# Optimization experiments

Hardware: AMD Instinct MI355X
Metric: run time of the kernel (lower is better)

The kernel has to match this reference:

```python
import jax, jax.numpy as jnp
import numpy as np
from jax import lax

H = 128       # hidden_size
N = 128       # total agents
T = 12        # future_steps (hardcoded by .view(12, ...))
K = 20        # num_modes
NHEADS = 4
HD = H // NHEADS
MIN_SCALE = 0.001


def setup_inputs() -> dict:
    key = jax.random.key(0)
    ks = jax.random.split(key, 48)

    def w(i, shape, fan):
        return (jax.random.normal(ks[i], shape, dtype=jnp.float32) / np.float32(np.sqrt(fan)))

    z = lambda *s: jnp.zeros(s, jnp.float32)
    o = lambda *s: jnp.ones(s, jnp.float32)
    inp = {}
    inp['global_embed'] = jax.random.normal(ks[0], (T, N, H), dtype=jnp.float32)
    inp['hidden_state'] = jax.random.normal(ks[1], (N, H), dtype=jnp.float32)
    inp['cn'] = jax.random.normal(ks[2], (N, H), dtype=jnp.float32)
    inp['shift_values'] = jax.random.normal(ks[3], (1, N, 2), dtype=jnp.float32)
    inp['max_values'] = jax.random.uniform(ks[4], (N, 2), dtype=jnp.float32)
    # multihead_proj_global: Linear(H, K*H) + LayerNorm + ReLU
    inp['mhp_W'] = w(5, (H, K * H), H); inp['mhp_b'] = z(K * H)
    inp['mhp_g'] = o(K * H); inp['mhp_beta'] = z(K * H)
    # two LSTMCells (bias = b_ih + b_hh fused)
    inp['lstm1_Wih'] = w(6, (H, 4 * H), H); inp['lstm1_Whh'] = w(7, (H, 4 * H), H); inp['lstm1_b'] = z(4 * H)
    inp['lstm2_Wih'] = w(8, (H, 4 * H), H); inp['lstm2_Whh'] = w(9, (H, 4 * H), H); inp['lstm2_b'] = z(4 * H)
    # MultiHeadSelfAttention
    inp['Wq'] = w(10, (H, H), H); inp['bq'] = z(H)
    inp['Wk'] = w(11, (H, H), H); inp['bk'] = z(H)
    inp['Wv'] = w(12, (H, H), H); inp['bv'] = z(H)
    inp['Wo1'] = w(13, (H, 2 * H), H); inp['bo1'] = z(2 * H)
    inp['Wo2'] = w(14, (2 * H, H), 2 * H); inp['bo2'] = z(H)
    # loc head: Linear + LN + ReLU + Linear(H,2)
    inp['loc_W1'] = w(15, (H, H), H); inp['loc_b1'] = z(H)
    inp['loc_g'] = o(H); inp['loc_beta'] = z(H)
    inp['loc_W2'] = w(16, (H, 2), H); inp['loc_b2'] = z(2)
    # scale head
    inp['scl_W1'] = w(17, (H, H), H); inp['scl_b1'] = z(H)
    inp['scl_g'] = o(H); inp['scl_beta'] = z(H)
    inp['scl_W2'] = w(18, (H, 2), H); inp['scl_b2'] = z(2)
    inp['batch_split'] = 4  # number of equal scene segments
    return inp


def _ln(x, g, b):
    m = jnp.mean(x, -1, keepdims=True)
    v = jnp.mean((x - m) ** 2, -1, keepdims=True)
    return (x - m) / jnp.sqrt(v + 1e-5) * g + b


def _head(x, W1, b1, g, beta, W2, b2):
    return jax.nn.relu(_ln(x @ W1 + b1, g, beta)) @ W2 + b2


def reference(global_embed, hidden_state, cn, shift_values, max_values,
              mhp_W, mhp_b, mhp_g, mhp_beta,
              lstm1_Wih, lstm1_Whh, lstm1_b,
              lstm2_Wih, lstm2_Whh, lstm2_b,
              Wq, bq, Wk, bk, Wv, bv, Wo1, bo1, Wo2, bo2,
              loc_W1, loc_b1, loc_g, loc_beta, loc_W2, loc_b2,
              scl_W1, scl_b1, scl_g, scl_beta, scl_W2, scl_b2,
              batch_split):
    S = int(batch_split)
    n = N // S
    # project global embed to per-mode embeddings: [T,N,K*H] -> [T,K*N,H] (mode-major)
    ge = jax.nn.relu(_ln(global_embed @ mhp_W + mhp_b, mhp_g, mhp_beta))
    ge = ge.reshape(T, N, K, H).transpose(0, 2, 1, 3).reshape(T, K * N, H)
    h0 = jnp.tile(hidden_state, (K, 1))  # [K*N,H]
    c0 = jnp.tile(cn, (K, 1))

    def cell1(carry, x):
        h, c = carry
        gi, gf, gg, go = jnp.split(x @ lstm1_Wih + h @ lstm1_Whh + lstm1_b, 4, -1)
        c2 = jax.nn.sigmoid(gf) * c + jax.nn.sigmoid(gi) * jnp.tanh(gg)
        h2 = jax.nn.sigmoid(go) * jnp.tanh(c2)
        return (h2, c2), h2

    _, output1 = lax.scan(cell1, (h0, c0), ge)  # [T,K*N,H]

    loc1 = _head(output1, loc_W1, loc_b1, loc_g, loc_beta, loc_W2, loc_b2)
    loc1 = loc1.transpose(1, 0, 2).reshape(K, N, T, 2)
    scale1 = jax.nn.elu(_head(output1, scl_W1, scl_b1, scl_g, scl_beta, scl_W2, scl_b2)) + 1.0 + MIN_SCALE
    scale1 = scale1.transpose(1, 0, 2).reshape(K, N, T, 2)

    sv = shift_values[0]  # squeeze(0) -> [N,2]
    loc1_ = loc1 * max_values[:, None, :] + sv[:, None, :]            # [K,N,T,2]
    loc1_ = loc1_.transpose(0, 2, 1, 3).reshape(K * T, N, 2).transpose(0, 2, 1)  # [K*T,2,N]
    locs = loc1_.reshape(K * T, 2, S, n).transpose(2, 0, 1, 3)        # [S,K*T,2,n]

    def split_mask(x):  # x: [K*T,2,n]
        d = jnp.abs(x[:, :, :, None] - x[:, :, None, :])              # [K*T,2,n,n]
        m = ((d[:, 0] < 10.0) & (d[:, 1] < 10.0)).reshape(K, T, n, n).any(0)  # [T,n,n]
        return jnp.tile(m, (1, K, K))                                  # [T,K*n,K*n]

    masks = jax.vmap(split_mask)(locs)  # [S,T,K*n,K*n]

    o1d = lax.stop_gradient(output1)  # detach, as in torch
    o1d = o1d.reshape(T, K, S, n, H).transpose(2, 0, 1, 3, 4).reshape(S, T, K * n, H)

    def mhsa(x, mask):  # x: [T,L,H], mask: [T,L,L] bool
        L = K * n
        q = (x @ Wq + bq).reshape(T, L, NHEADS, HD)
        k = (x @ Wk + bk).reshape(T, L, NHEADS, HD)
        v = (x @ Wv + bv).reshape(T, L, NHEADS, HD)
        s = jnp.einsum('blhd,bmhd->bhlm', q, k) / np.float32(np.sqrt(HD))
        s = jnp.where(mask[:, None], s, jnp.float32(-1e8))
        ctx = jnp.einsum('bhlm,bmhd->blhd', jax.nn.softmax(s, -1), v).reshape(T, L, H)
        return jax.nn.relu(ctx @ Wo1 + bo1) @ Wo2 + bo2

    social = jax.vmap(mhsa)(o1d, masks)                                # [S,T,K*n,H]
    social = social.reshape(S, T, K, n, H).transpose(1, 2, 0, 3, 4).reshape(T, K * N, H)

    def cell2(carry, xs):
        h, c = carry
        x, soc = xs
        c = c + soc
        h = h + jnp.tanh(c)
        gi, gf, gg, go = jnp.split(x @ lstm2_Wih + h @ lstm2_Whh + lstm2_b, 4, -1)
        c2 = jax.nn.sigmoid(gf) * c + jax.nn.sigmoid(gi) * jnp.tanh(gg)
        h2 = jax.nn.sigmoid(go) * jnp.tanh(c2)
        return (h2, c2), h2

    _, output2 = lax.scan(cell2, (h0, c0), (ge, social))  # [T,K*N,H]

    loc2 = _head(output2, loc_W1, loc_b1, loc_g, loc_beta, loc_W2, loc_b2)
    loc2 = loc2.transpose(1, 0, 2).reshape(K, N, T, 2)
    scale2 = jax.nn.elu(_head(output2, scl_W1, scl_b1, scl_g, scl_beta, scl_W2, scl_b2)) + 1.0 + MIN_SCALE
    scale2 = scale2.transpose(1, 0, 2).reshape(K, N, T, 2)

    return jnp.stack([loc1, scale1, loc2, scale2], 0)  # [4,K,N,T,2]
```

## Files before the change

kernel.cpp:

```cpp
#include <hip/hip_runtime.h>
#include <hip/hip_bf16.h>

typedef __hip_bfloat16 bf16_t;

static const int cT  = 12;
static const int cN  = 128;
static const int cH  = 128;
static const int cK  = 20;
static const int cKN = 2560;
static const int cS  = 4;
static const int cNS = 32;
static const int cL  = 640;
static const int cHD = 32;

#define CONV_TOTAL 977986

__constant__ int c_off[38] = {0,196608,212992,229376,229632,229888,557568,560128,562688,
  565248,630784,696320,696832,762368,827904,828416,844800,844928,861312,861440,877824,
  877952,910720,910976,943744,943872,960256,960384,960512,960640,960896,960960,977344,
  977472,977600,977728,977984,977986};
__constant__ int c_len[37] = {196608,16384,16384,256,256,327680,2560,2560,2560,
  65536,65536,512,65536,65536,512,16384,128,16384,128,16384,128,
  32768,256,32768,128,16384,128,128,128,256,2,16384,128,128,128,256,2};

struct Ptrs { const void* p[37]; };

typedef __attribute__((ext_vector_type(4))) float f32x4;
typedef __attribute__((ext_vector_type(8))) __bf16 bf16x8;

__device__ __forceinline__ float sigm(float x){ return 1.f/(1.f+expf(-x)); }
__device__ __forceinline__ unsigned short f2h(float x){ return (unsigned short)(__float_as_uint(x)>>16); }
__device__ __forceinline__ float hif(float x){ return __uint_as_float(__float_as_uint(x)&0xFFFF0000u); }

__global__ __launch_bounds__(256) void k_detect(const unsigned short* ge_u16, int* flagp, unsigned int* outw){
  __shared__ int cnt;
  if (threadIdx.x == 0) cnt = 0;
  __syncthreads();
  int ok = 0;
  for (int i = threadIdx.x; i < 128; i += 64){
    unsigned short u = ge_u16[2*i];
    int ex = (u >> 7) & 0xFF;
    if (ex >= 100 && ex <= 140) ok++;
  }
  atomicAdd(&cnt, ok);
  __syncthreads();
  if (threadIdx.x == 0){
    *flagp = (cnt >= 96) ? 1 : 0;
    outw[0] = 0x7FC07FC0u;
  }
}

__global__ __launch_bounds__(256) void k_convert(Ptrs ptrs, const int* flagp, float* dst){
  int g = blockIdx.x*256 + threadIdx.x;
  if (g >= CONV_TOTAL) return;
  int flag = *flagp;
  int seg = 0;
  while (seg < 36 && g >= c_off[seg+1]) ++seg;
  int local = g - c_off[seg];
  if (local >= c_len[seg]) return;
  float v;
  if (flag) v = __bfloat162float(((const bf16_t*)ptrs.p[seg])[local]);
  else      v = ((const float*)ptrs.p[seg])[local];
  dst[g] = v;
}

__global__ __launch_bounds__(256) void k_wprep3(const float* W, unsigned short* out){
  int idx = blockIdx.x*256 + threadIdx.x;
  int l = idx & 63;
  int rest = idx >> 6;
  int s = rest & 3;
  int n = rest >> 2;
  int g = l >> 4, c16 = l & 15;
  unsigned short hi[8], lo[8];
  #pragma unroll
  for (int e = 0; e < 8; ++e){
    int k = 32*s + 16*(e>>2) + 4*g + (e&3);
    float v = W[k*2560 + 16*n + c16];
    hi[e] = f2h(v); lo[e] = f2h(v - hif(v));
  }
  size_t base = (size_t)idx*8;
  *(uint4*)&out[base]          = *(const uint4*)hi;
  *(uint4*)&out[base + 327680] = *(const uint4*)lo;
}

__global__ __launch_bounds__(256) void k_mhp_ln(const float* y, const float* g,
                      const float* be, float* out){
  int row = blockIdx.x;
  int tid = threadIdx.x;
  __shared__ float red[256];
  float v[10];
  const float* yr = y + (size_t)row*2560;
  #pragma unroll
  for (int m = 0; m < 10; ++m) v[m] = yr[tid + 256*m];
  float ps = 0.f;
  #pragma unroll
  for (int m = 0; m < 10; ++m) ps += v[m];
  red[tid] = ps; __syncthreads();
  for (int s2 = 128; s2 > 0; s2 >>= 1){
    if (tid < s2) red[tid] += red[tid+s2];
    __syncthreads();
  }
  float mean = red[0]*(1.f/2560.f);
  __syncthreads();
  float pv = 0.f;
  #pragma unroll
  for (int m = 0; m < 10; ++m){ float d = v[m]-mean; pv += d*d; }
  red[tid] = pv; __syncthreads();
  for (int s2 = 128; s2 > 0; s2 >>= 1){
    if (tid < s2) red[tid] += red[tid+s2];
    __syncthreads();
  }
  float inv = rsqrtf(red[0]*(1.f/2560.f) + 1e-5f);
  int t = row >> 7, nn = row & 127;
  #pragma unroll
  for (int m = 0; m < 10; ++m){
    int col = tid + 256*m;
    float z = (v[m]-mean)*inv*g[col] + be[col];
    z = fmaxf(z, 0.f);
    int k = col >> 7, hh2 = col & 127;
    out[((t*cKN) + k*cN + nn)*cH + hh2] = z;
  }
}

__global__ __launch_bounds__(256) void k_wprep(const float* w0, const float* w1,
    const float* w2, const float* w3, unsigned short* out){
  int idx = blockIdx.x*256 + threadIdx.x;
  int m = idx >> 13;
  int rest = idx & 8191;
  int n = rest >> 8;
  int s = (rest >> 6) & 3;
  int l = rest & 63;
  int g = l >> 4, c16 = l & 15;
  const float* W = (m==0) ? w0 : ((m==1) ? w1 : ((m==2) ? w2 : w3));
  unsigned short hi[8], lo[8];
  #pragma unroll
  for (int e = 0; e < 8; ++e){
    int k = 32*s + 16*(e>>2) + 4*g + (e&3);
    float v = W[k*512 + 16*n + c16];
    hi[e] = f2h(v); lo[e] = f2h(v - hif(v));
  }
  size_t base = (size_t)m*131072 + (size_t)((n*4 + s)*64 + l)*8;
  *(uint4*)&out[base]         = *(const uint4*)hi;
  *(uint4*)&out[base + 65536] = *(const uint4*)lo;
}

__global__ __launch_bounds__(256) void k_wprep2(const float* wq, const float* wk,
    const float* wv, const float* wo1, const float* wo2,
    unsigned short* outA, unsigned short* outB){
  int idx = blockIdx.x*256 + threadIdx.x;
  if (idx >= 14336) return;
  const float* W; int KF, N, local, half; unsigned short* out; size_t off;
  if (idx < 2048)      { W=wq;  KF=4; N=128; off=0;      local=idx;       half=16384; out=outA; }
  else if (idx < 4096) { W=wk;  KF=4; N=128; off=32768;  local=idx-2048;  half=16384; out=outA; }
  else if (idx < 6144) { W=wv;  KF=4; N=128; off=65536;  local=idx-4096;  half=16384; out=outA; }
  else if (idx < 10240){ W=wo1; KF=4; N=256; off=98304;  local=idx-6144;  half=32768; out=outA; }
  else                 { W=wo2; KF=8; N=128; off=0;      local=idx-10240; half=32768; out=outB; }
  int l = local & 63;
  int rest = local >> 6;
  int s = rest & (KF-1);
  int n = (KF == 8) ? (rest >> 3) : (rest >> 2);
  int g = l >> 4, c16 = l & 15;
  unsigned short hi[8], lo[8];
  #pragma unroll
  for (int e = 0; e < 8; ++e){
    int k = 32*s + 16*(e>>2) + 4*g + (e&3);
    float v = W[k*N + 16*n + c16];
    hi[e] = f2h(v); lo[e] = f2h(v - hif(v));
  }
  size_t base = off + (size_t)local*8;
  *(uint4*)&out[base]        = *(const uint4*)hi;
  *(uint4*)&out[base + half] = *(const uint4*)lo;
}

__global__ __launch_bounds__(512) void k_lstm_mfma(const float* ge, float* outh,
    const float* hs0, const float* cn0, const float* soc,
    const unsigned short* wfA, const unsigned short* wfB,
    const float* bias, int phase){
  int r0 = blockIdx.x * 16;
  int tid = threadIdx.x;
  int w = tid >> 6, l = tid & 63;
  int g = l >> 4, c16 = l & 15;
  int scol = w*16 + c16;
  __shared__ unsigned short HFh[2][4][64][8], HFl[2][4][64][8];
  int ps = scol >> 5, prem = scol & 31;
  int pgf = (prem >> 2) & 3;
  int pe  = ((prem >> 4) << 2) + (prem & 3);
  float c[4], h[4];
  #pragma unroll
  for (int r = 0; r < 4; ++r){
    int nn = (r0 + 4*g + r) & 127;
    c[r] = cn0[nn*cH + scol];
    h[r] = hs0[nn*cH + scol];
  }
  float bias_t[4];
  #pragma unroll
  for (int tt = 0; tt < 4; ++tt) bias_t[tt] = bias[tt*128 + scol];

  f32x4 xr[8];
  float socr[4] = {0.f, 0.f, 0.f, 0.f};
  {
    const f32x4* gp = (const f32x4*)ge + ((size_t)(r0 + c16))*32;
    #pragma unroll
    for (int s = 0; s < 4; ++s){ xr[2*s] = gp[8*s + g]; xr[2*s+1] = gp[8*s + 4 + g]; }
    if (phase == 2){
      #pragma unroll
      for (int r = 0; r < 4; ++r)
        socr[r] = soc[(size_t)(r0 + 4*g + r)*cH + scol];
    }
  }

  for (int t = 0; t < cT; ++t){
    int b = t & 1;
    if (phase == 2){
      #pragma unroll
      for (int r = 0; r < 4; ++r){
        c[r] += socr[r];
        h[r] += tanhf(c[r]);
      }
    }
    #pragma unroll
    for (int r = 0; r < 4; ++r){
      HFh[b][ps][pgf*16 + 4*g + r][pe] = f2h(h[r]);
      HFl[b][ps][pgf*16 + 4*g + r][pe] = f2h(h[r] - hif(h[r]));
    }
    bf16x8 xh[4], xl[4];
    #pragma unroll
    for (int s = 0; s < 4; ++s){
      union { unsigned short u[8]; bf16x8 v; } uh, ul;
      #pragma unroll
      for (int m2 = 0; m2 < 4; ++m2){
        float a0 = xr[2*s][m2], b0 = xr[2*s+1][m2];
        uh.u[m2]   = f2h(a0); ul.u[m2]   = f2h(a0 - hif(a0));
        uh.u[4+m2] = f2h(b0); ul.u[4+m2] = f2h(b0 - hif(b0));
      }
      xh[s] = uh.v; xl[s] = ul.v;
    }
    if (t < cT-1){
      const f32x4* gp = (const f32x4*)ge + ((size_t)(t+1)*cKN + r0 + c16)*32;
      #pragma unroll
      for (int s = 0; s < 4; ++s){ xr[2*s] = gp[8*s + g]; xr[2*s+1] = gp[8*s + 4 + g]; }
      if (phase == 2){
        #pragma unroll
        for (int r = 0; r < 4; ++r)
          socr[r] = soc[(size_t)(t+1)*cKN*cH + (size_t)(r0 + 4*g + r)*cH + scol];
      }
    }
    __syncthreads();
    bf16x8 hh[4], hl[4];
    #pragma unroll
    for (int s = 0; s < 4; ++s){
      hh[s] = *(const bf16x8*)&HFh[b][s][l][0];
      hl[s] = *(const bf16x8*)&HFl[b][s][l][0];
    }
    f32x4 a4[4];
    #pragma unroll
    for (int tt = 0; tt < 4; ++tt){
      f32x4 acc = {bias_t[tt], bias_t[tt], bias_t[tt], bias_t[tt]};
      a4[tt] = acc;
    }
    {
      bf16x8 cAh, cAl, cBh, cBl, nAh, nAl, nBh, nBl;
      {
        size_t fo = (size_t)((w*4 + 0)*64 + l)*8;
        cAh = *(const bf16x8*)&wfA[fo];
        cAl = *(const bf16x8*)&wfA[65536 + fo];
        cBh = *(const bf16x8*)&wfB[fo];
        cBl = *(const bf16x8*)&wfB[65536 + fo];
      }
      #pragma unroll
      for (int j = 0; j < 16; ++j){
        int s = j >> 2, tt = j & 3;
        if (j < 15){
          int j2 = j + 1;
          int s2 = j2 >> 2, tt2 = j2 & 3;
          size_t fo = (size_t)(((w + 8*tt2)*4 + s2)*64 + l)*8;
          nAh = *(const bf16x8*)&wfA[fo];
          nAl = *(const bf16x8*)&wfA[65536 + fo];
          nBh = *(const bf16x8*)&wfB[fo];
          nBl = *(const bf16x8*)&wfB[65536 + fo];
        }
        f32x4 acc = a4[tt];
        acc = __builtin_amdgcn_mfma_f32_16x16x32_bf16(xl[s], cAh, acc, 0, 0, 0);
        acc = __builtin_amdgcn_mfma_f32_16x16x32_bf16(xh[s], cAl, acc, 0, 0, 0);
        acc = __builtin_amdgcn_mfma_f32_16x16x32_bf16(xh[s], cAh, acc, 0, 0, 0);
        acc = __builtin_amdgcn_mfma_f32_16x16x32_bf16(hl[s], cBh, acc, 0, 0, 0);
        acc = __builtin_amdgcn_mfma_f32_16x16x32_bf16(hh[s], cBl, acc, 0, 0, 0);
        acc = __builtin_amdgcn_mfma_f32_16x16x32_bf16(hh[s], cBh, acc, 0, 0, 0);
        a4[tt] = acc;
        cAh = nAh; cAl = nAl; cBh = nBh; cBl = nBl;
      }
    }
    #pragma unroll
    for (int r = 0; r < 4; ++r){
      float ig = sigm(a4[0][r]), fg = sigm(a4[1][r]);
      float gg = tanhf(a4[2][r]), og = sigm(a4[3][r]);
      c[r] = fg*c[r] + ig*gg;
      h[r] = og*tanhf(c[r]);
      outh[(size_t)t*cKN*cH + (size_t)(r0 + 4*g + r)*cH + scol] = h[r];
    }
  }
}

template<int KF>
__global__ __launch_bounds__(256) void k_gemm(const float* x, const unsigned short* wf,
    const float* bias, float* out, int NT, int N, int relu, int half, int ntc){
  int r0 = blockIdx.x * 16;
  int nt0 = blockIdx.y * ntc;
  int ntEnd = nt0 + ntc; if (ntEnd > NT) ntEnd = NT;
  int tid = threadIdx.x;
  int wv = tid >> 6, l = tid & 63;
  int g = l >> 4, c16 = l & 15;
  bf16x8 xh[KF], xl[KF];
  const f32x4* gp = (const f32x4*)x + (size_t)(r0 + c16)*(KF*8);
  #pragma unroll
  for (int s = 0; s < KF; ++s){
    f32x4 qa = gp[8*s + g], qb = gp[8*s + 4 + g];
    union { unsigned short u[8]; bf16x8 v; } uh, ul;
    #pragma unroll
    for (int m2 = 0; m2 < 4; ++m2){
      float a0 = qa[m2], b0 = qb[m2];
      uh.u[m2]   = f2h(a0); ul.u[m2]   = f2h(a0 - hif(a0));
      uh.u[4+m2] = f2h(b0); ul.u[4+m2] = f2h(b0 - hif(b0));
    }
    xh[s] = uh.v; xl[s] = ul.v;
  }
  for (int nt = nt0 + wv; nt < ntEnd; nt += 4){
    float bb = bias[nt*16 + c16];
    f32x4 acc = {bb, bb, bb, bb};
    #pragma unroll
    for (int s = 0; s < KF; ++s){
      const unsigned short* fb = wf + (size_t)((nt*KF + s)*64 + l)*8;
      bf16x8 Wh = *(const bf16x8*)fb;
      bf16x8 Wl = *(const bf16x8*)(fb + half);
      acc = __builtin_amdgcn_mfma_f32_16x16x32_bf16(xl[s], Wh, acc, 0, 0, 0);
      acc = __builtin_amdgcn_mfma_f32_16x16x32_bf16(xh[s], Wl, acc, 0, 0, 0);
      acc = __builtin_amdgcn_mfma_f32_16x16x32_bf16(xh[s], Wh, acc, 0, 0, 0);
    }
    if (relu){
      #pragma unroll
      for (int r = 0; r < 4; ++r) acc[r] = fmaxf(acc[r], 0.f);
    }
    #pragma unroll
    for (int r = 0; r < 4; ++r)
      out[(size_t)(r0 + 4*g + r)*N + nt*16 + c16] = acc[r];
  }
}

__global__ __launch_bounds__(256) void k_gemm3(const float* x, const unsigned short* wf,
    const float* bq, const float* bk, const float* bv,
    float* Q, float* K2, float* V){
  int r0 = blockIdx.x * 16;
  int tid = threadIdx.x;
  int wv = tid >> 6, l = tid & 63;
  int g = l >> 4, c16 = l & 15;
  bf16x8 xh[4], xl[4];
  const f32x4* gp = (const f32x4*)x + (size_t)(r0 + c16)*32;
  #pragma unroll
  for (int s = 0; s < 4; ++s){
    f32x4 qa = gp[8*s + g], qb = gp[8*s + 4 + g];
    union { unsigned short u[8]; bf16x8 v; } uh, ul;
    #pragma unroll
    for (int m2 = 0; m2 < 4; ++m2){
      float a0 = qa[m2], b0 = qb[m2];
      uh.u[m2]   = f2h(a0); ul.u[m2]   = f2h(a0 - hif(a0));
      uh.u[4+m2] = f2h(b0); ul.u[4+m2] = f2h(b0 - hif(b0));
    }
    xh[s] = uh.v; xl[s] = ul.v;
  }
  for (int nt = wv; nt < 24; nt += 4){
    int m = nt >> 3, n = nt & 7;
    const float* bias = (m==0) ? bq : ((m==1) ? bk : bv);
    float* out = (m==0) ? Q : ((m==1) ? K2 : V);
    float bb = bias[n*16 + c16];
    f32x4 acc = {bb, bb, bb, bb};
    const unsigned short* base = wf + (size_t)m*32768;
    #pragma unroll
    for (int s = 0; s < 4; ++s){
      const unsigned short* fb = base + (size_t)((n*4 + s)*64 + l)*8;
      bf16x8 Wh = *(const bf16x8*)fb;
      bf16x8 Wl = *(const bf16x8*)(fb + 16384);
      acc = __builtin_amdgcn_mfma_f32_16x16x32_bf16(xl[s], Wh, acc, 0, 0, 0);
      acc = __builtin_amdgcn_mfma_f32_16x16x32_bf16(xh[s], Wl, acc, 0, 0, 0);
      acc = __builtin_amdgcn_mfma_f32_16x16x32_bf16(xh[s], Wh, acc, 0, 0, 0);
    }
    #pragma unroll
    for (int r = 0; r < 4; ++r)
      out[(size_t)(r0 + 4*g + r)*cH + n*16 + c16] = acc[r];
  }
}

__global__ __launch_bounds__(256) void k_wo12(const float* x, const unsigned short* wf1,
    const float* b1, const unsigned short* wf2, const float* b2, float* out){
  int r0 = blockIdx.x * 16;
  int tid = threadIdx.x;
  int wv = tid >> 6, l = tid & 63;
  int g = l >> 4, c16 = l & 15;
  __shared__ unsigned short HFh[8][64][8], HFl[8][64][8];
  bf16x8 xh[4], xl[4];
  const f32x4* gp = (const f32x4*)x + (size_t)(r0 + c16)*32;
  #pragma unroll
  for (int s = 0; s < 4; ++s){
    f32x4 qa = gp[8*s + g], qb = gp[8*s + 4 + g];
    union { unsigned short u[8]; bf16x8 v; } uh, ul;
    #pragma unroll
    for (int m2 = 0; m2 < 4; ++m2){
      float a0 = qa[m2], b0v = qb[m2];
      uh.u[m2]   = f2h(a0);  ul.u[m2]   = f2h(a0 - hif(a0));
      uh.u[4+m2] = f2h(b0v); ul.u[4+m2] = f2h(b0v - hif(b0v));
    }
    xh[s] = uh.v; xl[s] = ul.v;
  }
  #pragma unroll
  for (int q = 0; q < 4; ++q){
    int nt = wv + 4*q;
    float bb = b1[nt*16 + c16];
    f32x4 acc = {bb, bb, bb, bb};
    #pragma unroll
    for (int s = 0; s < 4; ++s){
      const unsigned short* fb = wf1 + (size_t)((nt*4 + s)*64 + l)*8;
      bf16x8 Wh = *(const bf16x8*)fb;
      bf16x8 Wl = *(const bf16x8*)(fb + 32768);
      acc = __builtin_amdgcn_mfma_f32_16x16x32_bf16(xl[s], Wh, acc, 0, 0, 0);
      acc = __builtin_amdgcn_mfma_f32_16x16x32_bf16(xh[s], Wl, acc, 0, 0, 0);
      acc = __builtin_amdgcn_mfma_f32_16x16x32_bf16(xh[s], Wh, acc, 0, 0, 0);
    }
    int scol = nt*16 + c16;
    int ps = scol >> 5, prem = scol & 31;
    int pgf = (prem >> 2) & 3;
    int pe  = ((prem >> 4) << 2) + (prem & 3);
    #pragma unroll
    for (int r = 0; r < 4; ++r){
      float z = fmaxf(acc[r], 0.f);
      HFh[ps][pgf*16 + 4*g + r][pe] = f2h(z);
      HFl[ps][pgf*16 + 4*g + r][pe] = f2h(z - hif(z));
    }
  }
  __syncthreads();
  bf16x8 yh[8], yl[8];
  #pragma unroll
  for (int s = 0; s < 8; ++s){
    yh[s] = *(const bf16x8*)&HFh[s][l][0];
    yl[s] = *(const bf16x8*)&HFl[s][l][0];
  }
  #pragma unroll
  for (int q = 0; q < 2; ++q){
    int nt = wv + 4*q;
    float bb = b2[nt*16 + c16];
    f32x4 acc = {bb, bb, bb, bb};
    #pragma unroll
    for (int s = 0; s < 8; ++s){
      const unsigned short* fb = wf2 + (size_t)((nt*8 + s)*64 + l)*8;
      bf16x8 Wh = *(const bf16x8*)fb;
      bf16x8 Wl = *(const bf16x8*)(fb + 32768);
      acc = __builtin_amdgcn_mfma_f32_16x16x32_bf16(yl[s], Wh, acc, 0, 0, 0);
      acc = __builtin_amdgcn_mfma_f32_16x16x32_bf16(yh[s], Wl, acc, 0, 0, 0);
      acc = __builtin_amdgcn_mfma_f32_16x16x32_bf16(yh[s], Wh, acc, 0, 0, 0);
    }
    #pragma unroll
    for (int r = 0; r < 4; ++r)
      out[(size_t)(r0 + 4*g + r)*cH + nt*16 + c16] = acc[r];
  }
}

__global__ __launch_bounds__(256) void k_heads(const float* x,
  const float* lW1, const float* lb1, const float* lg, const float* lbe, const float* lW2, const float* lb2v,
  const float* sW1, const float* sb1, const float* sg, const float* sbe, const float* sW2, const float* sb2v,
  void* outv, int q0, float* locsc, const float* maxv, const float* svp, const int* flagp){
  const int ROWS = 16;
  int r0 = blockIdx.x*ROWS;
  __shared__ float xs[ROWS][cH];
  int tid = threadIdx.x;
  for (int p = tid; p < ROWS*32; p += 256){
    int rr = p>>5, u4 = p&31;
    ((float4*)&xs[rr][0])[u4] = ((const float4*)x)[(size_t)(r0+rr)*32 + u4];
  }
  __syncthreads();
  int wv = tid >> 6, lane = tid & 63;
  int head = wv & 1;
  int rbase = (wv >> 1)*8;
  const float* W1 = head ? sW1 : lW1;
  const float* b1 = head ? sb1 : lb1;
  const float* gv = head ? sg  : lg;
  const float* be = head ? sbe : lbe;
  const float* W2 = head ? sW2 : lW2;
  const float* b2 = head ? sb2v: lb2v;
  int j0 = lane, j1 = lane + 64;
  float b10 = b1[j0], b11 = b1[j1];
  float a0[8], a1[8];
  #pragma unroll
  for (int r = 0; r < 8; ++r){ a0[r] = b10; a1[r] = b11; }
  for (int i = 0; i < cH; ++i){
    float w0 = W1[i*cH + j0], w1 = W1[i*cH + j1];
    #pragma unroll
    for (int r = 0; r < 8; ++r){
      float xv = xs[rbase + r][i];
      a0[r] += xv*w0; a1[r] += xv*w1;
    }
  }
  float g0 = gv[j0], g1 = gv[j1], be0 = be[j0], be1 = be[j1];
  float w2a0 = W2[j0*2+0], w2a1 = W2[j0*2+1];
  float w2b0 = W2[j1*2+0], w2b1 = W2[j1*2+1];
  int flag = *flagp;
  float bias0 = b2[0], bias1 = b2[1];
  for (int r = 0; r < 8; ++r){
    float s = a0[r] + a1[r];
    #pragma unroll
    for (int off = 1; off < 64; off <<= 1) s += __shfl_xor(s, off);
    float mean = s*(1.f/128.f);
    float d0 = a0[r]-mean, d1 = a1[r]-mean;
    float vv = d0*d0 + d1*d1;
    #pragma unroll
    for (int off = 1; off < 64; off <<= 1) vv += __shfl_xor(vv, off);
    float inv = rsqrtf(vv*(1.f/128.f) + 1e-5f);
    float z0 = fmaxf(d0*inv*g0 + be0, 0.f);
    float z1 = fmaxf(d1*inv*g1 + be1, 0.f);
    float o0 = z0*w2a0 + z1*w2b0;
    float o1 = z0*w2a1 + z1*w2b1;
    #pragma unroll
    for (int off = 1; off < 64; off <<= 1){
      o0 += __shfl_xor(o0, off);
      o1 += __shfl_xor(o1, off);
    }
    if (lane == 0){
      int rg = r0 + rbase + r;
      int t = rg / cKN, rem = rg - t*cKN;
      int k = rem >> 7, nn = rem & 127;
      float u0 = o0 + bias0, u1 = o1 + bias1;
      if (head == 0){
        size_t oi = (((size_t)q0*cK + k)*cN + nn)*(cT*2) + t*2;
        if (flag){ ((bf16_t*)outv)[oi] = __float2bfloat16(u0); ((bf16_t*)outv)[oi+1] = __float2bfloat16(u1); }
        else     { ((float*)outv)[oi] = u0; ((float*)outv)[oi+1] = u1; }
        if (locsc){
          locsc[((size_t)t*cKN + rem)*2 + 0] = u0*maxv[nn*2+0] + svp[nn*2+0];
          locsc[((size_t)t*cKN + rem)*2 + 1] = u1*maxv[nn*2+1] + svp[nn*2+1];
        }
      } else {
        float e0 = (u0 > 0.f ? u0 : expm1f(u0)) + 1.001f;
        float e1 = (u1 > 0.f ? u1 : expm1f(u1)) + 1.001f;
        size_t oi = (((size_t)(q0+1)*cK + k)*cN + nn)*(cT*2) + t*2;
        if (flag){ ((bf16_t*)outv)[oi] = __float2bfloat16(e0); ((bf16_t*)outv)[oi+1] = __float2bfloat16(e1); }
        else     { ((float*)outv)[oi] = e0; ((float*)outv)[oi+1] = e1; }
      }
    }
  }
}

__global__ __launch_bounds__(256) void k_mask(const float* locsc, unsigned char* m){
  int st = blockIdx.x;
  int s = st / cT, t = st - s*cT;
  __shared__ float lx[cK][cNS], ly[cK][cNS];
  int tid = threadIdx.x;
  for (int p = tid; p < cK*cNS; p += 256){
    int k = p >> 5, i = p & 31;
    int row = t*cKN + k*cN + s*cNS + i;
    lx[k][i] = locsc[row*2+0];
    ly[k][i] = locsc[row*2+1];
  }
  __syncthreads();
  for (int p = tid; p < 1024; p += 256){
    int i = p >> 5, j = p & 31;
    bool any = false;
    for (int k = 0; k < cK; ++k){
      float dx = fabsf(lx[k][i]-lx[k][j]);
      float dy = fabsf(ly[k][i]-ly[k][j]);
      any = any || ((dx < 10.f) && (dy < 10.f));
    }
    m[st*1024 + p] = any ? 1 : 0;
  }
}

__global__ __launch_bounds__(256) void k_attn(const float* Q, const float* Kx, const float* V,
                       const unsigned char* msk, float* ctx){
  int qs   = blockIdx.x;
  int head = blockIdx.y;
  int st   = blockIdx.z;
  int s = st / cT, t = st - s*cT;
  __shared__ unsigned short KLh[2][1024], KLl[2][1024], VLh[2][1024], VLl[2][1024];
  int tid = threadIdx.x;
  int w = tid >> 6, lane = tid & 63;
  int g = lane >> 4, col = lane & 15;
  const float scl = 0.17677669529663687f;

  unsigned int mw0 = 0, mw1 = 0;
  {
    const unsigned int* mr0 = (const unsigned int*)(msk + st*1024 + col*32);
    const unsigned int* mr1 = (const unsigned int*)(msk + st*1024 + (16+col)*32);
    #pragma unroll
    for (int j2 = 0; j2 < 8; ++j2){
      mw0 |= (((mr0[j2] * 0x01020408u) >> 24) & 0xFu) << (4*j2);
      mw1 |= (((mr1[j2] * 0x01020408u) >> 24) & 0xFu) << (4*j2);
    }
  }

  bf16x8 Qh[2], Ql[2];
  int modes[2], ahs[2];
  #pragma unroll
  for (int i = 0; i < 2; ++i){
    int tt = qs*8 + 4*i + w;
    int mode = tt >> 1, ah = tt & 1;
    modes[i] = mode; ahs[i] = ah;
    int qrow = t*cKN + mode*cN + s*cNS + ah*16 + col;
    const f32x4* qp = (const f32x4*)Q + (size_t)qrow*32 + head*8;
    f32x4 qa = qp[g], qb = qp[4+g];
    union { unsigned short u[8]; bf16x8 v; } uh, ul;
    #pragma unroll
    for (int m = 0; m < 4; ++m){
      float x0 = qa[m]*scl;
      uh.u[m] = f2h(x0);
      ul.u[m] = f2h(x0 - hif(x0));
      float x1 = qb[m]*scl;
      uh.u[4+m] = f2h(x1);
      ul.u[4+m] = f2h(x1 - hif(x1));
    }
    Qh[i] = uh.v; Ql[i] = ul.v;
  }

  int kk = tid >> 3, f4 = tid & 7;
  int kwi = (((kk>>4)*4 + (f4&3))*16 + (kk&15))*8 + (f4>>2)*4;
  int vd = tid & 31, quad = tid >> 5;
  int vkey = (quad>>2)*16 + (quad&3)*4;
  int vwi = (((vd>>4)*4 + (quad&3))*16 + (vd&15))*8 + (quad>>2)*4;

  const size_t cstepK = (size_t)cN*32;
  const size_t cstepV = (size_t)cN*128;
  const float4* kptr = (const float4*)Kx + ((size_t)(t*cKN + s*cNS + kk))*32 + head*8 + f4;
  const float*  vptr = V + ((size_t)(t*cKN + s*cNS + vkey))*128 + head*32 + vd;

  float4 kv; float vm0, vm1, vm2, vm3;
  kv = *kptr; kptr += cstepK;
  vm0 = vptr[0]; vm1 = vptr[128]; vm2 = vptr[256]; vm3 = vptr[384]; vptr += cstepV;
  {
    unsigned int h0 = (unsigned int)f2h(kv.x) | ((unsigned int)f2h(kv.y)<<16);
    unsigned int h1 = (unsigned int)f2h(kv.z) | ((unsigned int)f2h(kv.w)<<16);
    float r0 = kv.x-hif(kv.x), r1 = kv.y-hif(kv.y), r2 = kv.z-hif(kv.z), r3 = kv.w-hif(kv.w);
    unsigned int l0 = (unsigned int)f2h(r0) | ((unsigned int)f2h(r1)<<16);
    unsigned int l1 = (unsigned int)f2h(r2) | ((unsigned int)f2h(r3)<<16);
    *(uint2*)&KLh[0][kwi] = make_uint2(h0,h1);
    *(uint2*)&KLl[0][kwi] = make_uint2(l0,l1);
    unsigned int vh0 = (unsigned int)f2h(vm0) | ((unsigned int)f2h(vm1)<<16);
    unsigned int vh1 = (unsigned int)f2h(vm2) | ((unsigned int)f2h(vm3)<<16);
    float s0 = vm0-hif(vm0), s1 = vm1-hif(vm1), s2 = vm2-hif(vm2), s3 = vm3-hif(vm3);
    unsigned int vl0 = (unsigned int)f2h(s0) | ((unsigned int)f2h(s1)<<16);
    unsigned int vl1 = (unsigned int)f2h(s2) | ((unsigned int)f2h(s3)<<16);
    *(uint2*)&VLh[0][vwi] = make_uint2(vh0,vh1);
    *(uint2*)&VLl[0][vwi] = make_uint2(vl0,vl1);
  }
  __syncthreads();

  const f32x4 Z = {0.f, 0.f, 0.f, 0.f};
  f32x4 O[2][2] = {{Z, Z}, {Z, Z}};
  float lac[2] = {0.f, 0.f};

  for (int ch = 0; ch < 20; ++ch){
    int par = ch & 1;
    if (ch < 19){
      kv = *kptr; kptr += cstepK;
      vm0 = vptr[0]; vm1 = vptr[128]; vm2 = vptr[256]; vm3 = vptr[384]; vptr += cstepV;
    }
    bf16x8 KAh0 = *(const bf16x8*)&KLh[par][( g      *16 + col)*8];
    bf16x8 KAl0 = *(const bf16x8*)&KLl[par][( g      *16 + col)*8];
    bf16x8 KAh1 = *(const bf16x8*)&KLh[par][((4 + g) *16 + col)*8];
    bf16x8 KAl1 = *(const bf16x8*)&KLl[par][((4 + g) *16 + col)*8];
    bf16x8 VBh0 = *(const bf16x8*)&VLh[par][( g      *16 + col)*8];
    bf16x8 VBl0 = *(const bf16x8*)&VLl[par][( g      *16 + col)*8];
    bf16x8 VBh1 = *(const bf16x8*)&VLh[par][((4 + g) *16 + col)*8];
    bf16x8 VBl1 = *(const bf16x8*)&VLl[par][((4 + g) *16 + col)*8];
    #pragma unroll
    for (int i = 0; i < 2; ++i){
      f32x4 sa = Z, sb = Z;
      sa = __builtin_amdgcn_mfma_f32_16x16x32_bf16(KAl0, Qh[i], sa, 0, 0, 0);
      sa = __builtin_amdgcn_mfma_f32_16x16x32_bf16(KAh0, Ql[i], sa, 0, 0, 0);
      sa = __builtin_amdgcn_mfma_f32_16x16x32_bf16(KAh0, Qh[i], sa, 0, 0, 0);
      sb = __builtin_amdgcn_mfma_f32_16x16x32_bf16(KAl1, Qh[i], sb, 0, 0, 0);
      sb = __builtin_amdgcn_mfma_f32_16x16x32_bf16(KAh1, Ql[i], sb, 0, 0, 0);
      sb = __builtin_amdgcn_mfma_f32_16x16x32_bf16(KAh1, Qh[i], sb, 0, 0, 0);
      unsigned int mw = ahs[i] ? mw1 : mw0;
      float p[8];
      #pragma unroll
      for (int r = 0; r < 4; ++r){
        float e0 = __expf(sa[r]);
        float e1 = __expf(sb[r]);
        p[r]   = ((mw >> (4*g + r)) & 1)        ? e0 : 0.f;
        p[4+r] = ((mw >> (16 + 4*g + r)) & 1)   ? e1 : 0.f;
      }
      lac[i] += ((p[0]+p[1])+(p[2]+p[3])) + ((p[4]+p[5])+(p[6]+p[7]));
      union { unsigned short u[8]; bf16x8 v; } Ph, Pl;
      #pragma unroll
      for (int e = 0; e < 8; ++e){
        Ph.u[e] = f2h(p[e]);
        Pl.u[e] = f2h(p[e] - hif(p[e]));
      }
      O[i][0] = __builtin_amdgcn_mfma_f32_16x16x32_bf16(Pl.v, VBh0, O[i][0], 0, 0, 0);
      O[i][0] = __builtin_amdgcn_mfma_f32_16x16x32_bf16(Ph.v, VBl0, O[i][0], 0, 0, 0);
      O[i][0] = __builtin_amdgcn_mfma_f32_16x16x32_bf16(Ph.v, VBh0, O[i][0], 0, 0, 0);
      O[i][1] = __builtin_amdgcn_mfma_f32_16x16x32_bf16(Pl.v, VBh1, O[i][1], 0, 0, 0);
      O[i][1] = __builtin_amdgcn_mfma_f32_16x16x32_bf16(Ph.v, VBl1, O[i][1], 0, 0, 0);
      O[i][1] = __builtin_amdgcn_mfma_f32_16x16x32_bf16(Ph.v, VBh1, O[i][1], 0, 0, 0);
    }
    __syncthreads();
    if (ch < 19){
      int nb = 1 - par;
      unsigned int h0 = (unsigned int)f2h(kv.x) | ((unsigned int)f2h(kv.y)<<16);
      unsigned int h1 = (unsigned int)f2h(kv.z) | ((unsigned int)f2h(kv.w)<<16);
      float r0 = kv.x-hif(kv.x), r1 = kv.y-hif(kv.y), r2 = kv.z-hif(kv.z), r3 = kv.w-hif(kv.w);
      unsigned int l0 = (unsigned int)f2h(r0) | ((unsigned int)f2h(r1)<<16);
      unsigned int l1 = (unsigned int)f2h(r2) | ((unsigned int)f2h(r3)<<16);
      *(uint2*)&KLh[nb][kwi] = make_uint2(h0,h1);
      *(uint2*)&KLl[nb][kwi] = make_uint2(l0,l1);
      unsigned int vh0 = (unsigned int)f2h(vm0) | ((unsigned int)f2h(vm1)<<16);
      unsigned int vh1 = (unsigned int)f2h(vm2) | ((unsigned int)f2h(vm3)<<16);
      float s0 = vm0-hif(vm0), s1 = vm1-hif(vm1), s2 = vm2-hif(vm2), s3 = vm3-hif(vm3);
      unsigned int vl0 = (unsigned int)f2h(s0) | ((unsigned int)f2h(s1)<<16);
      unsigned int vl1 = (unsigned int)f2h(s2) | ((unsigned int)f2h(s3)<<16);
      *(uint2*)&VLh[nb][vwi] = make_uint2(vh0,vh1);
      *(uint2*)&VLl[nb][vwi] = make_uint2(vl0,vl1);
    }
    __syncthreads();
  }

  #pragma unroll
  for (int i = 0; i < 2; ++i){
    float lsum = lac[i];
    lsum += __shfl_xor(lsum, 16);
    lsum += __shfl_xor(lsum, 32);
    int base = t*cKN + modes[i]*cN + s*cNS + ahs[i]*16;
    #pragma unroll
    for (int r = 0; r < 4; ++r){
      float lq = __shfl(lsum, 4*g + r);
      float rinv = 1.f / lq;
      float* cp = ctx + (size_t)(base + 4*g + r)*cH + head*cHD;
      cp[col]      = O[i][0][r] * rinv;
      cp[col+16]   = O[i][1][r] * rinv;
    }
  }
}

extern "C" void kernel_launch(void* const* d_in, const int* in_sizes, int n_in,
                              void* d_out, int out_size, void* d_ws, size_t ws_size,
                              hipStream_t stream){
  (void)in_sizes; (void)n_in; (void)out_size; (void)ws_size;

  int*   flagp = (int*)d_ws;
  float* conv  = (float*)d_ws + 64;
  float* big   = (float*)d_ws + 978112;

  const float* ge_f   = conv + 0;
  const float* hs_f   = conv + 196608;
  const float* cn_f   = conv + 212992;
  const float* sv_f   = conv + 229376;
  const float* mx_f   = conv + 229632;
  const float* mhpW_f = conv + 229888;
  const float* mhpb_f = conv + 557568;
  const float* mhpg_f = conv + 560128;
  const float* mhpbe_f= conv + 562688;
  const float* l1Wih_f= conv + 565248;
  const float* l1Whh_f= conv + 630784;
  const float* l1b_f  = conv + 696320;
  const float* l2Wih_f= conv + 696832;
  const float* l2Whh_f= conv + 762368;
  const float* l2b_f  = conv + 827904;
  const float* Wq_f   = conv + 828416;
  const float* bq_f   = conv + 844800;
  const float* Wk_f   = conv + 844928;
  const float* bk_f   = conv + 861312;
  const float* Wv_f   = conv + 861440;
  const float* bv_f   = conv + 877824;
  const float* Wo1_f  = conv + 877952;
  const float* bo1_f  = conv + 910720;
  const float* Wo2_f  = conv + 910976;
  const float* bo2_f  = conv + 943744;
  const float* locW1_f= conv + 943872;
  const float* locb1_f= conv + 960256;
  const float* locg_f = conv + 960384;
  const float* locbe_f= conv + 960512;
  const float* locW2_f= conv + 960640;
  const float* locb2_f= conv + 960896;
  const float* sclW1_f= conv + 960960;
  const float* sclb1_f= conv + 977344;
  const float* sclg_f = conv + 977472;
  const float* sclbe_f= conv + 977600;
  const float* sclW2_f= conv + 977728;
  const float* sclb2_f= conv + 977984;

  const size_t SLOT = (size_t)cT*cKN*cH;
  float* geb = big;
  float* o1b = big + SLOT;
  float* Qb  = big + 2*SLOT;
  float* Kb  = big + 3*SLOT;
  float* Vb  = big + 4*SLOT;
  float* locsc = big + 5*SLOT;
  unsigned char* maskb = (unsigned char*)(locsc + (size_t)cT*cKN*2);
  float* social = Vb;

  unsigned short* wfrag = (unsigned short*)(conv + 229888);
  unsigned short* uA = (unsigned short*)(conv + 565248);
  unsigned short* uB = (unsigned short*)(conv + 696832);
  unsigned short* mfrag = (unsigned short*)(big + 2*SLOT);
  float* ytmp = big + 3*SLOT;

  Ptrs ptrs;
  for (int i = 0; i < 37; ++i) ptrs.p[i] = d_in[i];

  k_detect<<<1, 64, 0, stream>>>((const unsigned short*)d_in[0], flagp, (unsigned int*)d_out);
  k_convert<<<(CONV_TOTAL+255)/256, 256, 0, stream>>>(ptrs, flagp, conv);
  k_wprep3<<<160, 256, 0, stream>>>(mhpW_f, mfrag);
  {
    dim3 mg(96, 5);
    k_gemm<4><<<mg, 256, 0, stream>>>(ge_f, mfrag, mhpb_f, ytmp, 160, 2560, 0, 327680, 32);
  }
  k_mhp_ln<<<1536, 256, 0, stream>>>(ytmp, mhpg_f, mhpbe_f, geb);
  k_wprep<<<128, 256, 0, stream>>>(l1Wih_f, l1Whh_f, l2Wih_f, l2Whh_f, wfrag);
  k_wprep2<<<56, 256, 0, stream>>>(Wq_f, Wk_f, Wv_f, Wo1_f, Wo2_f, uA, uB);
  k_lstm_mfma<<<160, 512, 0, stream>>>(geb, o1b, hs_f, cn_f, (const float*)0,
                                       wfrag + 0, wfrag + 131072, l1b_f, 1);
  k_heads<<<cT*cKN/16, 256, 0, stream>>>(o1b, locW1_f,locb1_f,locg_f,locbe_f,locW2_f,locb2_f,
                                        sclW1_f,sclb1_f,sclg_f,sclbe_f,sclW2_f,sclb2_f,
                                        d_out, 0, locsc, mx_f, sv_f, flagp);
  k_mask<<<cS*cT, 256, 0, stream>>>(locsc, maskb);
  k_gemm3<<<cT*cKN/16, 256, 0, stream>>>(o1b, uA, bq_f, bk_f, bv_f, Qb, Kb, Vb);
  {
    dim3 ag(5, 4, cS*cT);
    k_attn<<<ag, 256, 0, stream>>>(Qb, Kb, Vb, maskb, o1b);
  }
  k_wo12<<<cT*cKN/16, 256, 0, stream>>>(o1b, uA + 98304, bo1_f, uB, bo2_f, social);
  k_lstm_mfma<<<160, 512, 0, stream>>>(geb, o1b, hs_f, cn_f, social,
                                       wfrag + 262144, wfrag + 393216, l2b_f, 2);
  k_heads<<<cT*cKN/16, 256, 0, stream>>>(o1b, locW1_f,locb1_f,locg_f,locbe_f,locW2_f,locb2_f,
                                        sclW1_f,sclb1_f,sclg_f,sclbe_f,sclW2_f,sclb2_f,
                                        d_out, 2, (float*)0, mx_f, sv_f, flagp);
}
```

Before: 584.7 us.

## Move head first-layer GEMMs to split-bf16 MFMA with separate LayerNorm kernel

```diff
diff --git a/kernel.cpp b/kernel.cpp
--- a/kernel.cpp
+++ b/kernel.cpp
@@ -146,15 +146,18 @@
 
 __global__ __launch_bounds__(256) void k_wprep2(const float* wq, const float* wk,
     const float* wv, const float* wo1, const float* wo2,
+    const float* lw1, const float* sw1,
     unsigned short* outA, unsigned short* outB){
   int idx = blockIdx.x*256 + threadIdx.x;
-  if (idx >= 14336) return;
+  if (idx >= 18432) return;
   const float* W; int KF, N, local, half; unsigned short* out; size_t off;
   if (idx < 2048)      { W=wq;  KF=4; N=128; off=0;      local=idx;       half=16384; out=outA; }
   else if (idx < 4096) { W=wk;  KF=4; N=128; off=32768;  local=idx-2048;  half=16384; out=outA; }
   else if (idx < 6144) { W=wv;  KF=4; N=128; off=65536;  local=idx-4096;  half=16384; out=outA; }
   else if (idx < 10240){ W=wo1; KF=4; N=256; off=98304;  local=idx-6144;  half=32768; out=outA; }
-  else                 { W=wo2; KF=8; N=128; off=0;      local=idx-10240; half=32768; out=outB; }
+  else if (idx < 14336){ W=wo2; KF=8; N=128; off=0;      local=idx-10240; half=32768; out=outB; }
+  else if (idx < 16384){ W=lw1; KF=4; N=128; off=163840; local=idx-14336; half=16384; out=outA; }
+  else                 { W=sw1; KF=4; N=128; off=196608; local=idx-16384; half=16384; out=outA; }
   int l = local & 63;
   int rest = local >> 6;
   int s = rest & (KF-1);
@@ -389,13 +392,12 @@
   }
 }
 
-__global__ __launch_bounds__(256) void k_wo12(const float* x, const unsigned short* wf1,
-    const float* b1, const unsigned short* wf2, const float* b2, float* out){
+__global__ __launch_bounds__(256) void k_heads_gemm(const float* x, const unsigned short* wf,
+    const float* bl, const float* bs, float* y){
   int r0 = blockIdx.x * 16;
   int tid = threadIdx.x;
   int wv = tid >> 6, l = tid & 63;
   int g = l >> 4, c16 = l & 15;
-  __shared__ unsigned short HFh[8][64][8], HFl[8][64][8];
   bf16x8 xh[4], xl[4];
   const f32x4* gp = (const f32x4*)x + (size_t)(r0 + c16)*32;
   #pragma unroll
@@ -404,129 +406,89 @@
     union { unsigned short u[8]; bf16x8 v; } uh, ul;
     #pragma unroll
     for (int m2 = 0; m2 < 4; ++m2){
-      float a0 = qa[m2], b0v = qb[m2];
-      uh.u[m2]   = f2h(a0);  ul.u[m2]   = f2h(a0 - hif(a0));
-      uh.u[4+m2] = f2h(b0v); ul.u[4+m2] = f2h(b0v - hif(b0v));
+      float a0 = qa[m2], b0 = qb[m2];
+      uh.u[m2]   = f2h(a0); ul.u[m2]   = f2h(a0 - hif(a0));
+      uh.u[4+m2] = f2h(b0); ul.u[4+m2] = f2h(b0 - hif(b0));
     }
     xh[s] = uh.v; xl[s] = ul.v;
   }
-  #pragma unroll
-  for (int q = 0; q < 4; ++q){
-    int nt = wv + 4*q;
-    float bb = b1[nt*16 + c16];
+  for (int nt = wv; nt < 16; nt += 4){
+    int m = nt >> 3, n = nt & 7;
+    const float* bias = m ? bs : bl;
+    float bb = bias[n*16 + c16];
     f32x4 acc = {bb, bb, bb, bb};
+    const unsigned short* base = wf + (size_t)m*32768;
     #pragma unroll
     for (int s = 0; s < 4; ++s){
-      const unsigned short* fb = wf1 + (size_t)((nt*4 + s)*64 + l)*8;
+      const unsigned short* fb = base + (size_t)((n*4 + s)*64 + l)*8;
       bf16x8 Wh = *(const bf16x8*)fb;
-      bf16x8 Wl = *(const bf16x8*)(fb + 32768);
+      bf16x8 Wl = *(const bf16x8*)(fb + 16384);
       acc = __builtin_amdgcn_mfma_f32_16x16x32_bf16(xl[s], Wh, acc, 0, 0, 0);
       acc = __builtin_amdgcn_mfma_f32_16x16x32_bf16(xh[s], Wl, acc, 0, 0, 0);
       acc = __builtin_amdgcn_mfma_f32_16x16x32_bf16(xh[s], Wh, acc, 0, 0, 0);
     }
-    int scol = nt*16 + c16;
-    int ps = scol >> 5, prem = scol & 31;
-    int pgf = (prem >> 2) & 3;
-    int pe  = ((prem >> 4) << 2) + (prem & 3);
-    #pragma unroll
-    for (int r = 0; r < 4; ++r){
-      float z = fmaxf(acc[r], 0.f);
-      HFh[ps][pgf*16 + 4*g + r][pe] = f2h(z);
-      HFl[ps][pgf*16 + 4*g + r][pe] = f2h(z - hif(z));
-    }
-  }
-  __syncthreads();
-  bf16x8 yh[8], yl[8];
-  #pragma unroll
-  for (int s = 0; s < 8; ++s){
-    yh[s] = *(const bf16x8*)&HFh[s][l][0];
-    yl[s] = *(const bf16x8*)&HFl[s][l][0];
-  }
-  #pragma unroll
-  for (int q = 0; q < 2; ++q){
-    int nt = wv + 4*q;
-    float bb = b2[nt*16 + c16];
-    f32x4 acc = {bb, bb, bb, bb};
-    #pragma unroll
-    for (int s = 0; s < 8; ++s){
-      const unsigned short* fb = wf2 + (size_t)((nt*8 + s)*64 + l)*8;
-      bf16x8 Wh = *(const bf16x8*)fb;
-      bf16x8 Wl = *(const bf16x8*)(fb + 32768);
-      acc = __builtin_amdgcn_mfma_f32_16x16x32_bf16(yl[s], Wh, acc, 0, 0, 0);
-      acc = __builtin_amdgcn_mfma_f32_16x16x32_bf16(yh[s], Wl, acc, 0, 0, 0);
-      acc = __builtin_amdgcn_mfma_f32_16x16x32_bf16(yh[s], Wh, acc, 0, 0, 0);
-    }
     #pragma unroll
     for (int r = 0; r < 4; ++r)
-      out[(size_t)(r0 + 4*g + r)*cH + nt*16 + c16] = acc[r];
-  }
-}
-
-__global__ __launch_bounds__(256) void k_heads(const float* x,
-  const float* lW1, const float* lb1, const float* lg, const float* lbe, const float* lW2, const float* lb2v,
-  const float* sW1, const float* sb1, const float* sg, const float* sbe, const float* sW2, const float* sb2v,
+      y[(size_t)(r0 + 4*g + r)*256 + m*128 + n*16 + c16] = acc[r];
+  }
+}
+
+__global__ __launch_bounds__(256) void k_heads_ln(const float* y,
+  const float* lg, const float* lbe, const float* lW2, const float* lb2v,
+  const float* sg, const float* sbe, const float* sW2, const float* sb2v,
   void* outv, int q0, float* locsc, const float* maxv, const float* svp, const int* flagp){
-  const int ROWS = 16;
-  int r0 = blockIdx.x*ROWS;
-  __shared__ float xs[ROWS][cH];
   int tid = threadIdx.x;
-  for (int p = tid; p < ROWS*32; p += 256){
-    int rr = p>>5, u4 = p&31;
-    ((float4*)&xs[rr][0])[u4] = ((const float4*)x)[(size_t)(r0+rr)*32 + u4];
-  }
-  __syncthreads();
   int wv = tid >> 6, lane = tid & 63;
-  int head = wv & 1;
-  int rbase = (wv >> 1)*8;
-  const float* W1 = head ? sW1 : lW1;
-  const float* b1 = head ? sb1 : lb1;
-  const float* gv = head ? sg  : lg;
-  const float* be = head ? sbe : lbe;
-  const float* W2 = head ? sW2 : lW2;
-  const float* b2 = head ? sb2v: lb2v;
   int j0 = lane, j1 = lane + 64;
-  float b10 = b1[j0], b11 = b1[j1];
-  float a0[8], a1[8];
-  #pragma unroll
-  for (int r = 0; r < 8; ++r){ a0[r] = b10; a1[r] = b11; }
-  for (int i = 0; i < cH; ++i){
-    float w0 = W1[i*cH + j0], w1 = W1[i*cH + j1];
-    #pragma unroll
-    for (int r = 0; r < 8; ++r){
-      float xv = xs[rbase + r][i];
-      a0[r] += xv*w0; a1[r] += xv*w1;
-    }
-  }
-  float g0 = gv[j0], g1 = gv[j1], be0 = be[j0], be1 = be[j1];
-  float w2a0 = W2[j0*2+0], w2a1 = W2[j0*2+1];
-  float w2b0 = W2[j1*2+0], w2b1 = W2[j1*2+1];
+  float lg0 = lg[j0], lg1 = lg[j1], lbe0 = lbe[j0], lbe1 = lbe[j1];
+  float sg0 = sg[j0], sg1 = sg[j1], sbe0 = sbe[j0], sbe1 = sbe[j1];
+  float lw2a0 = lW2[j0*2+0], lw2a1 = lW2[j0*2+1];
+  float lw2b0 = lW2[j1*2+0], lw2b1 = lW2[j1*2+1];
+  float sw2a0 = sW2[j0*2+0], sw2a1 = sW2[j0*2+1];
+  float sw2b0 = sW2[j1*2+0], sw2b1 = sW2[j1*2+1];
   int flag = *flagp;
-  float bias0 = b2[0], bias1 = b2[1];
+  float lb20 = lb2v[0], lb21 = lb2v[1], sb20 = sb2v[0], sb21 = sb2v[1];
   for (int r = 0; r < 8; ++r){
-    float s = a0[r] + a1[r];
-    #pragma unroll
-    for (int off = 1; off < 64; off <<= 1) s += __shfl_xor(s, off);
-    float mean = s*(1.f/128.f);
-    float d0 = a0[r]-mean, d1 = a1[r]-mean;
-    float vv = d0*d0 + d1*d1;
-    #pragma unroll
-    for (int off = 1; off < 64; off <<= 1) vv += __shfl_xor(vv, off);
-    float inv = rsqrtf(vv*(1.f/128.f) + 1e-5f);
-    float z0 = fmaxf(d0*inv*g0 + be0, 0.f);
-    float z1 = fmaxf(d1*inv*g1 + be1, 0.f);
-    float o0 = z0*w2a0 + z1*w2b0;
-    float o1 = z0*w2a1 + z1*w2b1;
+    int rg = blockIdx.x*32 + wv*8 + r;
+    const float* yr = y + (size_t)rg*256;
+    float a0 = yr[j0], a1 = yr[j1];
+    float c0 = yr[128+j0], c1 = yr[128+j1];
+    float sl = a0 + a1, ss = c0 + c1;
+    #pragma unroll
+    for (int off = 1; off < 64; off <<= 1){
+      sl += __shfl_xor(sl, off);
+      ss += __shfl_xor(ss, off);
+    }
+    float ml = sl*(1.f/128.f), ms = ss*(1.f/128.f);
+    float d0 = a0-ml, d1 = a1-ml, e0v = c0-ms, e1v = c1-ms;
+    float vl = d0*d0 + d1*d1, vs = e0v*e0v + e1v*e1v;
+    #pragma unroll
+    for (int off = 1; off < 64; off <<= 1){
+      vl += __shfl_xor(vl, off);
+      vs += __shfl_xor(vs, off);
+    }
+    float il = rsqrtf(vl*(1.f/128.f) + 1e-5f);
+    float is = rsqrtf(vs*(1.f/128.f) + 1e-5f);
+    float z0 = fmaxf(d0*il*lg0 + lbe0, 0.f);
+    float z1 = fmaxf(d1*il*lg1 + lbe1, 0.f);
+    float y0 = fmaxf(e0v*is*sg0 + sbe0, 0.f);
+    float y1 = fmaxf(e1v*is*sg1 + sbe1, 0.f);
+    float o0 = z0*lw2a0 + z1*lw2b0;
+    float o1 = z0*lw2a1 + z1*lw2b1;
+    float p0 = y0*sw2a0 + y1*sw2b0;
+    float p1 = y0*sw2a1 + y1*sw2b1;
     #pragma unroll
     for (int off = 1; off < 64; off <<= 1){
       o0 += __shfl_xor(o0, off);
       o1 += __shfl_xor(o1, off);
+      p0 += __shfl_xor(p0, off);
+      p1 += __shfl_xor(p1, off);
     }
     if (lane == 0){
-      int rg = r0 + rbase + r;
       int t = rg / cKN, rem = rg - t*cKN;
       int k = rem >> 7, nn = rem & 127;
-      float u0 = o0 + bias0, u1 = o1 + bias1;
-      if (head == 0){
+      float u0 = o0 + lb20, u1 = o1 + lb21;
+      {
         size_t oi = (((size_t)q0*cK + k)*cN + nn)*(cT*2) + t*2;
         if (flag){ ((bf16_t*)outv)[oi] = __float2bfloat16(u0); ((bf16_t*)outv)[oi+1] = __float2bfloat16(u1); }
         else     { ((float*)outv)[oi] = u0; ((float*)outv)[oi+1] = u1; }
@@ -534,9 +496,11 @@
           locsc[((size_t)t*cKN + rem)*2 + 0] = u0*maxv[nn*2+0] + svp[nn*2+0];
           locsc[((size_t)t*cKN + rem)*2 + 1] = u1*maxv[nn*2+1] + svp[nn*2+1];
         }
-      } else {
-        float e0 = (u0 > 0.f ? u0 : expm1f(u0)) + 1.001f;
-        float e1 = (u1 > 0.f ? u1 : expm1f(u1)) + 1.001f;
+      }
+      {
+        float w0 = p0 + sb20, w1 = p1 + sb21;
+        float e0 = (w0 > 0.f ? w0 : expm1f(w0)) + 1.001f;
+        float e1 = (w1 > 0.f ? w1 : expm1f(w1)) + 1.001f;
         size_t oi = (((size_t)(q0+1)*cK + k)*cN + nn)*(cT*2) + t*2;
         if (flag){ ((bf16_t*)outv)[oi] = __float2bfloat16(e0); ((bf16_t*)outv)[oi+1] = __float2bfloat16(e1); }
         else     { ((float*)outv)[oi] = e0; ((float*)outv)[oi+1] = e1; }
@@ -566,6 +530,79 @@
       any = any || ((dx < 10.f) && (dy < 10.f));
     }
     m[st*1024 + p] = any ? 1 : 0;
+  }
+}
+
+__global__ __launch_bounds__(256) void k_wo12(const float* x, const unsigned short* wf1,
+    const float* b1, const unsigned short* wf2, const float* b2, float* out){
+  int r0 = blockIdx.x * 16;
+  int tid = threadIdx.x;
+  int wv = tid >> 6, l = tid & 63;
+  int g = l >> 4, c16 = l & 15;
+  __shared__ unsigned short HFh[8][64][8], HFl[8][64][8];
+  bf16x8 xh[4], xl[4];
+  const f32x4* gp = (const f32x4*)x + (size_t)(r0 + c16)*32;
+  #pragma unroll
+  for (int s = 0; s < 4; ++s){
+    f32x4 qa = gp[8*s + g], qb = gp[8*s + 4 + g];
+    union { unsigned short u[8]; bf16x8 v; } uh, ul;
+    #pragma unroll
+    for (int m2 = 0; m2 < 4; ++m2){
+      float a0 = qa[m2], b0v = qb[m2];
+      uh.u[m2]   = f2h(a0);  ul.u[m2]   = f2h(a0 - hif(a0));
+      uh.u[4+m2] = f2h(b0v); ul.u[4+m2] = f2h(b0v - hif(b0v));
+    }
+    xh[s] = uh.v; xl[s] = ul.v;
+  }
+  #pragma unroll
+  for (int q = 0; q < 4; ++q){
+    int nt = wv + 4*q;
+    float bb = b1[nt*16 + c16];
+    f32x4 acc = {bb, bb, bb, bb};
+    #pragma unroll
+    for (int s = 0; s < 4; ++s){
+      const unsigned short* fb = wf1 + (size_t)((nt*4 + s)*64 + l)*8;
+      bf16x8 Wh = *(const bf16x8*)fb;
+      bf16x8 Wl = *(const bf16x8*)(fb + 32768);
+      acc = __builtin_amdgcn_mfma_f32_16x16x32_bf16(xl[s], Wh, acc, 0, 0, 0);
+      acc = __builtin_amdgcn_mfma_f32_16x16x32_bf16(xh[s], Wl, acc, 0, 0, 0);
+      acc = __builtin_amdgcn_mfma_f32_16x16x32_bf16(xh[s], Wh, acc, 0, 0, 0);
+    }
+    int scol = nt*16 + c16;
+    int ps = scol >> 5, prem = scol & 31;
+    int pgf = (prem >> 2) & 3;
+    int pe  = ((prem >> 4) << 2) + (prem & 3);
+    #pragma unroll
+    for (int r = 0; r < 4; ++r){
+      float z = fmaxf(acc[r], 0.f);
+      HFh[ps][pgf*16 + 4*g + r][pe] = f2h(z);
+      HFl[ps][pgf*16 + 4*g + r][pe] = f2h(z - hif(z));
+    }
+  }
+  __syncthreads();
+  bf16x8 yh[8], yl[8];
+  #pragma unroll
+  for (int s = 0; s < 8; ++s){
+    yh[s] = *(const bf16x8*)&HFh[s][l][0];
+    yl[s] = *(const bf16x8*)&HFl[s][l][0];
+  }
+  #pragma unroll
+  for (int q = 0; q < 2; ++q){
+    int nt = wv + 4*q;
+    float bb = b2[nt*16 + c16];
+    f32x4 acc = {bb, bb, bb, bb};
+    #pragma unroll
+    for (int s = 0; s < 8; ++s){
+      const unsigned short* fb = wf2 + (size_t)((nt*8 + s)*64 + l)*8;
+      bf16x8 Wh = *(const bf16x8*)fb;
+      bf16x8 Wl = *(const bf16x8*)(fb + 32768);
+      acc = __builtin_amdgcn_mfma_f32_16x16x32_bf16(yl[s], Wh, acc, 0, 0, 0);
+      acc = __builtin_amdgcn_mfma_f32_16x16x32_bf16(yh[s], Wl, acc, 0, 0, 0);
+      acc = __builtin_amdgcn_mfma_f32_16x16x32_bf16(yh[s], Wh, acc, 0, 0, 0);
+    }
+    #pragma unroll
+    for (int r = 0; r < 4; ++r)
+      out[(size_t)(r0 + 4*g + r)*cH + nt*16 + c16] = acc[r];
   }
 }
 
@@ -797,6 +834,7 @@
   unsigned short* uB = (unsigned short*)(conv + 696832);
   unsigned short* mfrag = (unsigned short*)(big + 2*SLOT);
   float* ytmp = big + 3*SLOT;
+  float* yhd  = big + 2*SLOT;
 
   Ptrs ptrs;
   for (int i = 0; i < 37; ++i) ptrs.p[i] = d_in[i];
@@ -810,11 +848,12 @@
   }
   k_mhp_ln<<<1536, 256, 0, stream>>>(ytmp, mhpg_f, mhpbe_f, geb);
   k_wprep<<<128, 256, 0, stream>>>(l1Wih_f, l1Whh_f, l2Wih_f, l2Whh_f, wfrag);
-  k_wprep2<<<56, 256, 0, stream>>>(Wq_f, Wk_f, Wv_f, Wo1_f, Wo2_f, uA, uB);
+  k_wprep2<<<72, 256, 0, stream>>>(Wq_f, Wk_f, Wv_f, Wo1_f, Wo2_f, locW1_f, sclW1_f, uA, uB);
   k_lstm_mfma<<<160, 512, 0, stream>>>(geb, o1b, hs_f, cn_f, (const float*)0,
                                        wfrag + 0, wfrag + 131072, l1b_f, 1);
-  k_heads<<<cT*cKN/16, 256, 0, stream>>>(o1b, locW1_f,locb1_f,locg_f,locbe_f,locW2_f,locb2_f,
-                                        sclW1_f,sclb1_f,sclg_f,sclbe_f,sclW2_f,sclb2_f,
+  k_heads_gemm<<<cT*cKN/16, 256, 0, stream>>>(o1b, uA + 163840, locb1_f, sclb1_f, yhd);
+  k_heads_ln<<<cT*cKN/32, 256, 0, stream>>>(yhd, locg_f, locbe_f, locW2_f, locb2_f,
+                                        sclg_f, sclbe_f, sclW2_f, sclb2_f,
                                         d_out, 0, locsc, mx_f, sv_f, flagp);
   k_mask<<<cS*cT, 256, 0, stream>>>(locsc, maskb);
   k_gemm3<<<cT*cKN/16, 256, 0, stream>>>(o1b, uA, bq_f, bk_f, bv_f, Qb, Kb, Vb);
@@ -825,7 +864,8 @@
   k_wo12<<<cT*cKN/16, 256, 0, stream>>>(o1b, uA + 98304, bo1_f, uB, bo2_f, social);
   k_lstm_mfma<<<160, 512, 0, stream>>>(geb, o1b, hs_f, cn_f, social,
                                        wfrag + 262144, wfrag + 393216, l2b_f, 2);
-  k_heads<<<cT*cKN/16, 256, 0, stream>>>(o1b, locW1_f,locb1_f,locg_f,locbe_f,locW2_f,locb2_f,
-                                        sclW1_f,sclb1_f,sclg_f,sclbe_f,sclW2_f,sclb2_f,
+  k_heads_gemm<<<cT*cKN/16, 256, 0, stream>>>(o1b, uA + 163840, locb1_f, sclb1_f, yhd);
+  k_heads_ln<<<cT*cKN/32, 256, 0, stream>>>(yhd, locg_f, locbe_f, locW2_f, locb2_f,
+                                        sclg_f, sclbe_f, sclW2_f, sclb2_f,
                                         d_out, 2, (float*)0, mx_f, sv_f, flagp);
 }
```

Measured after the change: 561.2 us, median of 2. -4.0%, faster.
